# Kernel optimization log

Measured on AMD Instinct MI355X. Metric: run time of the kernel, lower is better.

The kernel has to match this reference:

```python
import jax
import jax.numpy as jnp
import numpy as np
from jax import lax

TAU = 1.0
EPS = 1e-20


def setup_inputs() -> dict:
    key = jax.random.key(0)
    ks = jax.random.split(key, 8)
    B, n, M, G = 256, 128, 512, 512  # batch, seq, mem_size, global dim
    SLOTS = 15                        # his_mem slots (mem_slots - 1)
    d_q = M + G
    his_mem = jax.random.normal(ks[0], (B, SLOTS, M), dtype=jnp.float32)
    states = jax.random.normal(ks[1], (B, n, M), dtype=jnp.float32)
    states_mask = jnp.round(jax.random.uniform(ks[2], (B, n), dtype=jnp.float32))
    global_trace = jax.random.normal(ks[3], (B, G), dtype=jnp.float32)
    null_mem = jnp.zeros((B, 1, M), dtype=jnp.float32)
    gumbel_u = jax.random.uniform(ks[4], (B, n, SLOTS + 1), dtype=jnp.float32)
    attn_W = jax.random.normal(ks[5], (M, d_q + M), dtype=jnp.float32) * 0.02
    attn_b = jax.random.normal(ks[6], (M,), dtype=jnp.float32) * 0.02
    stdv = 1.0 / np.sqrt(M)
    v = jax.random.normal(ks[7], (M,), dtype=jnp.float32) * stdv
    return {"his_mem": his_mem, "states": states, "states_mask": states_mask,
            "global_trace": global_trace, "null_mem": null_mem,
            "gumbel_u": gumbel_u, "attn_W": attn_W, "attn_b": attn_b, "v": v}


def _gumbel_softmax_hard(logits, u, tau):
    # deterministic gumbel noise from uniform samples u in [0,1)
    g = -jnp.log(-jnp.log(jnp.clip(u, EPS, 1.0)) + EPS)
    y_soft = jax.nn.softmax((logits + g) / tau, axis=-1)
    y_hard = jax.nn.one_hot(jnp.argmax(y_soft, axis=-1), logits.shape[-1],
                            dtype=y_soft.dtype)
    # straight-through estimator (matches torch F.gumbel_softmax hard=True)
    return y_hard - lax.stop_gradient(y_soft) + y_soft


def _forward(his_mem, states, states_mask, global_trace, null_mem,
             gumbel_u, attn_W, attn_b, v):
    B, n, M = states.shape
    S = his_mem.shape[1] + 1  # mem_slots (including null slot)

    def step(hm, xs):
        state, mask, u = xs  # [B,M], [B], [B,S]
        mem = jnp.concatenate([hm, null_mem], axis=1)          # [B,S,M]
        query = jnp.concatenate([state, global_trace], axis=1)  # [B,d_q]
        q = jnp.broadcast_to(query[:, None, :], (B, S, query.shape[-1]))
        energy = jnp.tanh(jnp.concatenate([q, mem], axis=2) @ attn_W.T + attn_b)
        attn_energies = energy @ v                              # [B,S]
        attn_weights = jax.nn.softmax(attn_energies, axis=-1)
        empty_mask = (jnp.sum(jnp.abs(mem), axis=-1) == 0).astype(attn_weights.dtype)
        attn_weights = attn_weights + empty_mask * 10.0
        slot_select = _gumbel_softmax_hard(attn_weights, u, TAU)  # [B,S]
        write_mask = (slot_select[:, : S - 1] * mask[:, None])[:, :, None]  # [B,S-1,1]
        hm = (1.0 - write_mask) * hm + write_mask * state[:, None, :]
        return hm, slot_select

    xs = (jnp.swapaxes(states, 0, 1),        # [n,B,M]
          jnp.swapaxes(states_mask, 0, 1),   # [n,B]
          jnp.swapaxes(gumbel_u, 0, 1))      # [n,B,S]
    hm_final, log = lax.scan(step, his_mem, xs)
    write_log = jnp.swapaxes(log, 0, 1)      # [B,n,S]
    return hm_final, write_log


def reference(his_mem, states, states_mask, global_trace, null_mem,
              gumbel_u, attn_W, attn_b, v):
    return _forward(his_mem, states, states_mask, global_trace, null_mem,
                    gumbel_u, attn_W, attn_b, v)
```

## Files before the change

kernel.cpp:

```cpp
#include <hip/hip_runtime.h>

constexpr int kB = 256;
constexpr int kN = 128;
constexpr int kM = 512;
constexpr int kSlots = 15;
constexpr int kS = 16;
constexpr int kW = 1536;
constexpr int kCap = 8192;

__device__ __forceinline__ float tanh_fast(float x)
{
    float xc = fminf(15.f, fmaxf(-15.f, x));
    float ex = __expf(2.f * xc);
    return 1.f - 2.f * __builtin_amdgcn_rcpf(ex + 1.f);
}

__global__ __launch_bounds__(256) void prep1_k(
    const float* __restrict__ his_mem, const float* __restrict__ null_mem,
    const float* __restrict__ gumbel_u, float* __restrict__ out,
    int* __restrict__ empty0, int* __restrict__ cnt, int* __restrict__ total,
    unsigned* __restrict__ list, int* __restrict__ listPos,
    int* __restrict__ ambBatch, unsigned char* __restrict__ amb_flags)
{
    const int b = blockIdx.x;
    const int tid = threadIdx.x;
    const int wave = tid >> 6, lane = tid & 63;
    __shared__ int eflag[kS];
    float* out_hm = out;
    float* out_log = out + (size_t)kB * kSlots * kM;

    for (int s = wave; s < kS; s += 4) {
        const float* p = (s < kSlots) ? his_mem + (size_t)(b * kSlots + s) * kM
                                      : null_mem + (size_t)b * kM;
        float4 v0 = *(const float4*)(p + lane * 4);
        float4 v1 = *(const float4*)(p + 256 + lane * 4);
        int nz = (v0.x != 0.f) | (v0.y != 0.f) | (v0.z != 0.f) | (v0.w != 0.f) |
                 (v1.x != 0.f) | (v1.y != 0.f) | (v1.z != 0.f) | (v1.w != 0.f);
        unsigned long long bal = __ballot(nz);
        if (lane == 0) eflag[s] = (bal == 0ull) ? 1 : 0;
        if (s < kSlots) {
            float* dst = out_hm + (size_t)(b * kSlots + s) * kM;
            *(float4*)(dst + lane * 4) = v0;
            *(float4*)(dst + 256 + lane * 4) = v1;
        }
    }
    __syncthreads();
    if (tid < kS) empty0[b * kS + tid] = eflag[tid];

    if (tid < kN) {
        const int idx = b * kN + tid;
        const float* up = gumbel_u + (size_t)idx * kS;
        float g[kS];
#pragma unroll
        for (int s = 0; s < kS; ++s) {
            float u = fminf(fmaxf(up[s], 1e-20f), 1.0f);
            g[s] = -logf(-logf(u) + 1e-20f);
        }
        float rhs = g[15] + 10.f * (eflag[15] ? 1.f : 0.f) - 1.01f;
        bool amb = false;
#pragma unroll
        for (int s = 0; s < kSlots; ++s)
            amb = amb || (g[s] + 10.f * (eflag[s] ? 1.f : 0.f) >= rhs);
        amb_flags[idx] = amb ? 1 : 0;
        if (amb) {
            int pos = atomicAdd(&total[0], 1);
            if (pos < kCap) list[pos] = (unsigned)idx;
            listPos[idx] = pos;
            int prev = atomicAdd(&cnt[b], 1);
            if (prev == 0) {
                int bp = atomicAdd(&total[1], 1);
                ambBatch[bp] = b;
            }
        }
        float* lp = out_log + (size_t)idx * kS;
        float4 zz = make_float4(0.f, 0.f, 0.f, 0.f);
        *(float4*)(lp + 0) = zz;
        *(float4*)(lp + 4) = zz;
        *(float4*)(lp + 8) = zz;
        *(float4*)(lp + 12) = make_float4(0.f, 0.f, 0.f, 1.f);
    }
}

__global__ __launch_bounds__(256) void prep2_k(
    const float* __restrict__ W, const float* __restrict__ his_mem,
    const float* __restrict__ null_mem, const float* __restrict__ states,
    const float* __restrict__ global_trace, const float* __restrict__ attn_b,
    const int* __restrict__ total, const int* __restrict__ ambBatch,
    const unsigned* __restrict__ list, float* __restrict__ C0,
    float* __restrict__ qCache, float* __restrict__ cwCache,
    int* __restrict__ stepNz)
{
    const int tid = threadIdx.x;

    if (blockIdx.x < 512) {
        const int nab = total[1];
        const int cx = blockIdx.x >> 3;
        const int cy = blockIdx.x & 7;
        if (cx * 4 >= nab) return;
        __shared__ float As[16 * 68];
        __shared__ float Bs[16 * 68];
        const int n0 = cy * 64;
        const int row_l = tid >> 2;
        const int k4 = (tid & 3) * 4;
        const int ty = tid >> 4, tx = tid & 15;

        int bi = cx * 4 + (row_l >> 4);
        if (bi >= nab) bi = nab - 1;
        const int b = ambBatch[bi];
        const int s = row_l & 15;
        const float* ap = (s < kSlots) ? (his_mem + (size_t)(b * kSlots + s) * kM)
                                       : (null_mem + (size_t)b * kM);
        const float* wp = W + (size_t)(n0 + row_l) * kW + 1024;

        float acc[4][4];
#pragma unroll
        for (int i = 0; i < 4; ++i)
#pragma unroll
            for (int j = 0; j < 4; ++j) acc[i][j] = 0.f;

        for (int kt = 0; kt < kM; kt += 16) {
            float4 a4 = *(const float4*)(ap + kt + k4);
            float4 b4 = *(const float4*)(wp + kt + k4);
            __syncthreads();
            As[(k4 + 0) * 68 + row_l] = a4.x; As[(k4 + 1) * 68 + row_l] = a4.y;
            As[(k4 + 2) * 68 + row_l] = a4.z; As[(k4 + 3) * 68 + row_l] = a4.w;
            Bs[(k4 + 0) * 68 + row_l] = b4.x; Bs[(k4 + 1) * 68 + row_l] = b4.y;
            Bs[(k4 + 2) * 68 + row_l] = b4.z; Bs[(k4 + 3) * 68 + row_l] = b4.w;
            __syncthreads();
#pragma unroll
            for (int k = 0; k < 16; ++k) {
                const float4 av = *(const float4*)&As[k * 68 + ty * 4];
                const float4 bv = *(const float4*)&Bs[k * 68 + tx * 4];
                acc[0][0] = fmaf(av.x, bv.x, acc[0][0]);
                acc[0][1] = fmaf(av.x, bv.y, acc[0][1]);
                acc[0][2] = fmaf(av.x, bv.z, acc[0][2]);
                acc[0][3] = fmaf(av.x, bv.w, acc[0][3]);
                acc[1][0] = fmaf(av.y, bv.x, acc[1][0]);
                acc[1][1] = fmaf(av.y, bv.y, acc[1][1]);
                acc[1][2] = fmaf(av.y, bv.z, acc[1][2]);
                acc[1][3] = fmaf(av.y, bv.w, acc[1][3]);
                acc[2][0] = fmaf(av.z, bv.x, acc[2][0]);
                acc[2][1] = fmaf(av.z, bv.y, acc[2][1]);
                acc[2][2] = fmaf(av.z, bv.z, acc[2][2]);
                acc[2][3] = fmaf(av.z, bv.w, acc[2][3]);
                acc[3][0] = fmaf(av.w, bv.x, acc[3][0]);
                acc[3][1] = fmaf(av.w, bv.y, acc[3][1]);
                acc[3][2] = fmaf(av.w, bv.z, acc[3][2]);
                acc[3][3] = fmaf(av.w, bv.w, acc[3][3]);
            }
        }
#pragma unroll
        for (int i = 0; i < 4; ++i) {
            int rl = ty * 4 + i;
            int bij = cx * 4 + (rl >> 4);
            if (bij >= nab) bij = nab - 1;
            int ro = ambBatch[bij] * kS + (rl & 15);
            float4 o = make_float4(acc[i][0], acc[i][1], acc[i][2], acc[i][3]);
            *(float4*)(C0 + (size_t)ro * kM + n0 + tx * 4) = o;
        }
    } else {
        int n = total[0];
        if (n > kCap) n = kCap;
        __shared__ float Xs[1024];
        __shared__ int nzs;

        for (int c = (int)blockIdx.x - 512; c < n * 16; c += 2048) {
            const int i = c >> 4;
            const int j = c & 15;
            const int idx = (int)list[i];
            const int b = idx >> 7;
            __syncthreads();
            if (tid == 0) nzs = 0;
            __syncthreads();
            float s0 = states[(size_t)idx * kM + tid];
            float s1 = states[(size_t)idx * kM + 256 + tid];
            Xs[tid] = s0; Xs[256 + tid] = s1;
            Xs[512 + tid] = global_trace[(size_t)b * kM + tid];
            Xs[768 + tid] = global_trace[(size_t)b * kM + 256 + tid];
            if (s0 != 0.f || s1 != 0.f) nzs = 1;
            __syncthreads();

            const int g = tid >> 4;
            const int l = tid & 15;
#pragma unroll
            for (int p = 0; p < 2; ++p) {
                const int r = j * 32 + p * 16 + g;
                const float* wr = W + (size_t)r * kW;
                float accq = 0.f, accc = 0.f;
#pragma unroll
                for (int jj = 0; jj < 16; ++jj) {
                    int k = l * 4 + jj * 64;
                    float4 w4 = *(const float4*)(wr + k);
                    float4 x4 = *(const float4*)&Xs[k];
                    accq = fmaf(w4.x, x4.x, accq); accq = fmaf(w4.y, x4.y, accq);
                    accq = fmaf(w4.z, x4.z, accq); accq = fmaf(w4.w, x4.w, accq);
                }
#pragma unroll
                for (int jj = 0; jj < 8; ++jj) {
                    int k = l * 4 + jj * 64;
                    float4 w4 = *(const float4*)(wr + 1024 + k);
                    float4 x4 = *(const float4*)&Xs[k];
                    accc = fmaf(w4.x, x4.x, accc); accc = fmaf(w4.y, x4.y, accc);
                    accc = fmaf(w4.z, x4.z, accc); accc = fmaf(w4.w, x4.w, accc);
                }
                accq += __shfl_xor(accq, 1); accq += __shfl_xor(accq, 2);
                accq += __shfl_xor(accq, 4); accq += __shfl_xor(accq, 8);
                accc += __shfl_xor(accc, 1); accc += __shfl_xor(accc, 2);
                accc += __shfl_xor(accc, 4); accc += __shfl_xor(accc, 8);
                if (l == 0) {
                    qCache[(size_t)i * kM + r] = accq + attn_b[r];
                    cwCache[(size_t)i * kM + r] = accc;
                }
            }
            if (tid == 0 && j == 0) stepNz[i] = nzs;
        }
    }
}

constexpr int kCsStride = 528;

__global__ __launch_bounds__(256) void phaseB_k(
    const float* __restrict__ C0, const int* __restrict__ empty0,
    const unsigned char* __restrict__ amb_flags, const int* __restrict__ cnt,
    const int* __restrict__ listPos, const float* __restrict__ qCache,
    const float* __restrict__ cwCache, const int* __restrict__ stepNz,
    const float* __restrict__ states, const float* __restrict__ states_mask,
    const float* __restrict__ gumbel_u, const float* __restrict__ global_trace,
    const float* __restrict__ W, const float* __restrict__ attn_b,
    const float* __restrict__ v, float* __restrict__ out)
{
    const int b = blockIdx.x;
    if (cnt[b] == 0) return;
    const int tid = threadIdx.x;
    float* out_hm = out;
    float* out_log = out + (size_t)kB * kSlots * kM;

    __shared__ float Cs[kS * kCsStride];
    __shared__ float Xb[1024];
    __shared__ float Qb[kM];
    __shared__ float vs[kM];
    __shared__ float e_sh[kS];
    __shared__ float empty_sh[kS];
    __shared__ unsigned char flS[kN];
    __shared__ int slot_src[kSlots];
    __shared__ int k_sh, wk_sh, nz_sh;

    for (int i = tid; i < kS * kM; i += 256) {
        int s = i >> 9, m = i & 511;
        Cs[s * kCsStride + m] = C0[(size_t)(b * kS + s) * kM + m];
    }
    for (int i = tid; i < kM; i += 256) {
        vs[i] = v[i];
        Xb[512 + i] = global_trace[(size_t)b * kM + i];
    }
    if (tid < kS) empty_sh[tid] = empty0[b * kS + tid] ? 1.0f : 0.0f;
    if (tid < kSlots) slot_src[tid] = -1;
    if (tid < kN) flS[tid] = amb_flags[b * kN + tid];
    __syncthreads();

    const int sidx = tid >> 4;
    const int ml = tid & 15;

    for (int t = 0; t < kN; ++t) {
        if (!flS[t]) continue;

        const int pos = listPos[b * kN + t];
        const float* qp;
        if (pos < kCap) {
            qp = qCache + (size_t)pos * kM;
        } else {
            Xb[tid] = states[(size_t)(b * kN + t) * kM + tid];
            Xb[256 + tid] = states[(size_t)(b * kN + t) * kM + 256 + tid];
            __syncthreads();
            const int g2 = tid >> 4, l2 = tid & 15;
            for (int r0 = 0; r0 < kM; r0 += 16) {
                int r = r0 + g2;
                const float* wr = W + (size_t)r * kW;
                float a = 0.f;
                for (int k = l2 * 4; k < 1024; k += 64) {
                    float4 w4 = *(const float4*)(wr + k);
                    float4 x4 = *(const float4*)&Xb[k];
                    a = fmaf(w4.x, x4.x, a); a = fmaf(w4.y, x4.y, a);
                    a = fmaf(w4.z, x4.z, a); a = fmaf(w4.w, x4.w, a);
                }
                a += __shfl_xor(a, 1); a += __shfl_xor(a, 2);
                a += __shfl_xor(a, 4); a += __shfl_xor(a, 8);
                if (l2 == 0) Qb[r] = a + attn_b[r];
            }
            __syncthreads();
            qp = Qb;
        }

        const float* crow = &Cs[sidx * kCsStride];
        float acc = 0.f;
#pragma unroll
        for (int j = 0; j < 8; ++j) {
            int m = ml * 4 + j * 64;
            float4 q4 = *(const float4*)(qp + m);
            float4 c4 = *(const float4*)&crow[m];
            float4 v4 = *(const float4*)&vs[m];
            acc = fmaf(v4.x, tanh_fast(q4.x + c4.x), acc);
            acc = fmaf(v4.y, tanh_fast(q4.y + c4.y), acc);
            acc = fmaf(v4.z, tanh_fast(q4.z + c4.z), acc);
            acc = fmaf(v4.w, tanh_fast(q4.w + c4.w), acc);
        }
        acc += __shfl_xor(acc, 1); acc += __shfl_xor(acc, 2);
        acc += __shfl_xor(acc, 4); acc += __shfl_xor(acc, 8);
        if (ml == 0) e_sh[sidx] = acc;
        __syncthreads();

        if (tid < 64) {
            int s = tid;
            float ev = (s < kS) ? e_sh[s] : -3.0e38f;
            float mx = ev;
            mx = fmaxf(mx, __shfl_xor(mx, 1));
            mx = fmaxf(mx, __shfl_xor(mx, 2));
            mx = fmaxf(mx, __shfl_xor(mx, 4));
            mx = fmaxf(mx, __shfl_xor(mx, 8));
            float w = (s < kS) ? __expf(ev - mx) : 0.f;
            float sm = w;
            sm += __shfl_xor(sm, 1); sm += __shfl_xor(sm, 2);
            sm += __shfl_xor(sm, 4); sm += __shfl_xor(sm, 8);
            w = w / sm;
            w += 10.0f * ((s < kS) ? empty_sh[s] : 0.f);
            float z;
            if (s < kS) {
                float u = gumbel_u[(size_t)(b * kN + t) * kS + s];
                u = fminf(fmaxf(u, 1e-20f), 1.0f);
                float g = -logf(-logf(u) + 1e-20f);
                z = w + g;
            } else z = -3.0e38f;
            float zm = z;
            zm = fmaxf(zm, __shfl_xor(zm, 1));
            zm = fmaxf(zm, __shfl_xor(zm, 2));
            zm = fmaxf(zm, __shfl_xor(zm, 4));
            zm = fmaxf(zm, __shfl_xor(zm, 8));
            unsigned long long bal = __ballot(z == zm) & 0xFFFFull;
            if (s == 0) k_sh = __ffsll(bal) - 1;
        }
        __syncthreads();

        const int k = k_sh;
        if (tid < kS) out_log[(size_t)(b * kN + t) * kS + tid] = (tid == k) ? 1.f : 0.f;
        if (tid == 0) {
            float mv = states_mask[b * kN + t];
            wk_sh = (k < kSlots && mv != 0.0f) ? k : -1;
            nz_sh = 0;
        }
        __syncthreads();

        const int wk = wk_sh;
        if (wk >= 0) {
            if (pos < kCap) {
                Cs[wk * kCsStride + tid] = cwCache[(size_t)pos * kM + tid];
                Cs[wk * kCsStride + 256 + tid] = cwCache[(size_t)pos * kM + 256 + tid];
                if (tid == 0) {
                    slot_src[wk] = t;
                    empty_sh[wk] = stepNz[pos] ? 0.f : 1.f;
                }
            } else {
                if (Xb[tid] != 0.f || Xb[256 + tid] != 0.f) nz_sh = 1;
                __syncthreads();
                const int g2 = tid >> 4, l2 = tid & 15;
                for (int r0 = 0; r0 < kM; r0 += 16) {
                    int r = r0 + g2;
                    const float* wr = W + (size_t)r * kW + 1024;
                    float ca = 0.f;
                    for (int k2 = l2 * 4; k2 < kM; k2 += 64) {
                        float4 w4 = *(const float4*)(wr + k2);
                        float4 x4 = *(const float4*)&Xb[k2];
                        ca = fmaf(w4.x, x4.x, ca); ca = fmaf(w4.y, x4.y, ca);
                        ca = fmaf(w4.z, x4.z, ca); ca = fmaf(w4.w, x4.w, ca);
                    }
                    ca += __shfl_xor(ca, 1); ca += __shfl_xor(ca, 2);
                    ca += __shfl_xor(ca, 4); ca += __shfl_xor(ca, 8);
                    if (l2 == 0) Cs[wk * kCsStride + r] = ca;
                }
                __syncthreads();
                if (tid == 0) {
                    slot_src[wk] = t;
                    empty_sh[wk] = nz_sh ? 0.f : 1.f;
                }
            }
        }
        __syncthreads();
    }

    for (int s = 0; s < kSlots; ++s) {
        int ts = slot_src[s];
        if (ts >= 0) {
            float* dst = out_hm + (size_t)(b * kSlots + s) * kM;
            dst[tid] = states[(size_t)(b * kN + ts) * kM + tid];
            dst[tid + 256] = states[(size_t)(b * kN + ts) * kM + tid + 256];
        }
    }
}

extern "C" void kernel_launch(void* const* d_in, const int* in_sizes, int n_in,
                              void* d_out, int out_size, void* d_ws, size_t ws_size,
                              hipStream_t stream)
{
    const float* his_mem      = (const float*)d_in[0];
    const float* states       = (const float*)d_in[1];
    const float* states_mask  = (const float*)d_in[2];
    const float* global_trace = (const float*)d_in[3];
    const float* null_mem     = (const float*)d_in[4];
    const float* gumbel_u     = (const float*)d_in[5];
    const float* attn_W       = (const float*)d_in[6];
    const float* attn_b       = (const float*)d_in[7];
    const float* v            = (const float*)d_in[8];

    float* C0 = (float*)d_ws;
    float* qCache = C0 + (size_t)kB * kS * kM;
    float* cwCache = qCache + (size_t)kCap * kM;
    int* cnt = (int*)(cwCache + (size_t)kCap * kM);
    int* total = cnt + kB;
    int* empty0 = total + 16;
    int* ambBatch = empty0 + kB * kS;
    int* stepNz = ambBatch + kB;
    int* listPos = stepNz + kCap;
    unsigned* list = (unsigned*)(listPos + kB * kN);
    unsigned char* amb = (unsigned char*)(list + kB * kN);

    hipMemsetAsync(cnt, 0, (kB + 16) * sizeof(int), stream);
    prep1_k<<<kB, 256, 0, stream>>>(his_mem, null_mem, gumbel_u, (float*)d_out,
                                    empty0, cnt, total, list, listPos, ambBatch,
                                    amb);
    prep2_k<<<2560, 256, 0, stream>>>(attn_W, his_mem, null_mem, states,
                                      global_trace, attn_b, total, ambBatch,
                                      list, C0, qCache, cwCache, stepNz);
    phaseB_k<<<kB, 256, 0, stream>>>(C0, empty0, amb, cnt, listPos, qCache,
                                     cwCache, stepNz, states, states_mask,
                                     gumbel_u, global_trace, attn_W, attn_b, v,
                                     (float*)d_out);
}
```

Baseline: 170.4 us.

## Fuse three kernels into one persistent kernel with grid barriers

```diff
diff --git a/kernel.cpp b/kernel.cpp
--- a/kernel.cpp
+++ b/kernel.cpp
@@ -7,6 +7,10 @@
 constexpr int kS = 16;
 constexpr int kW = 1536;
 constexpr int kCap = 8192;
+constexpr int kMaxA = 128;
+constexpr int kGrid = 512;
+constexpr int kCsStride = 528;
+constexpr int kBarStride = 16;
 
 __device__ __forceinline__ float tanh_fast(float x)
 {
@@ -15,169 +19,236 @@
     return 1.f - 2.f * __builtin_amdgcn_rcpf(ex + 1.f);
 }
 
-__global__ __launch_bounds__(256) void prep1_k(
-    const float* __restrict__ his_mem, const float* __restrict__ null_mem,
-    const float* __restrict__ gumbel_u, float* __restrict__ out,
-    int* __restrict__ empty0, int* __restrict__ cnt, int* __restrict__ total,
-    unsigned* __restrict__ list, int* __restrict__ listPos,
-    int* __restrict__ ambBatch, unsigned char* __restrict__ amb_flags)
+__device__ __forceinline__ void grid_barrier(unsigned* bar, unsigned phase)
 {
-    const int b = blockIdx.x;
+    __syncthreads();
+    if (threadIdx.x < 64) {
+        if (threadIdx.x == 0) {
+            __threadfence();
+            atomicAdd(&bar[(blockIdx.x & 63) * kBarStride], 1u);
+        }
+        const unsigned tgt = phase * (kGrid / 64);
+        while (__hip_atomic_load(&bar[threadIdx.x * kBarStride],
+                                 __ATOMIC_RELAXED, __HIP_MEMORY_SCOPE_AGENT) < tgt)
+            __builtin_amdgcn_s_sleep(2);
+        __threadfence();
+    }
+    __syncthreads();
+}
+
+__global__ __launch_bounds__(256, 2) void fused_k(
+    const float* __restrict__ his_mem, const float* __restrict__ states,
+    const float* __restrict__ states_mask, const float* __restrict__ global_trace,
+    const float* __restrict__ null_mem, const float* __restrict__ gumbel_u,
+    const float* __restrict__ W, const float* __restrict__ attn_b,
+    const float* __restrict__ v, float* __restrict__ out, float* __restrict__ C0,
+    float* __restrict__ qCache, float* __restrict__ cwCache,
+    int* __restrict__ cnt_g, int* __restrict__ ambT_g, int* __restrict__ stepNz,
+    unsigned* __restrict__ bar)
+{
     const int tid = threadIdx.x;
-    const int wave = tid >> 6, lane = tid & 63;
-    __shared__ int eflag[kS];
+    const int bid = blockIdx.x;
+
+    __shared__ __align__(16) float SCR[10496];
+    __shared__ float empty_p[kS];
+    __shared__ unsigned char ambList_p[kMaxA];
+    __shared__ int Pex_p[kB + 1];
+    __shared__ short ambBatch_p[kB];
+    __shared__ int wcnt_p[2];
+    __shared__ int cntLoc_p, nab_p, T_p, Pb_p;
+    __shared__ float e_sh[kS];
+    __shared__ int slot_src[kSlots];
+    __shared__ int k_sh, wk_sh, nz_sh;
+
     float* out_hm = out;
     float* out_log = out + (size_t)kB * kSlots * kM;
 
-    for (int s = wave; s < kS; s += 4) {
-        const float* p = (s < kSlots) ? his_mem + (size_t)(b * kSlots + s) * kM
-                                      : null_mem + (size_t)b * kM;
-        float4 v0 = *(const float4*)(p + lane * 4);
-        float4 v1 = *(const float4*)(p + 256 + lane * 4);
-        int nz = (v0.x != 0.f) | (v0.y != 0.f) | (v0.z != 0.f) | (v0.w != 0.f) |
-                 (v1.x != 0.f) | (v1.y != 0.f) | (v1.z != 0.f) | (v1.w != 0.f);
-        unsigned long long bal = __ballot(nz);
-        if (lane == 0) eflag[s] = (bal == 0ull) ? 1 : 0;
-        if (s < kSlots) {
-            float* dst = out_hm + (size_t)(b * kSlots + s) * kM;
-            *(float4*)(dst + lane * 4) = v0;
-            *(float4*)(dst + 256 + lane * 4) = v1;
-        }
-    }
-    __syncthreads();
-    if (tid < kS) empty0[b * kS + tid] = eflag[tid];
-
-    if (tid < kN) {
-        const int idx = b * kN + tid;
-        const float* up = gumbel_u + (size_t)idx * kS;
-        float g[kS];
-#pragma unroll
-        for (int s = 0; s < kS; ++s) {
-            float u = fminf(fmaxf(up[s], 1e-20f), 1.0f);
-            g[s] = -logf(-logf(u) + 1e-20f);
-        }
-        float rhs = g[15] + 10.f * (eflag[15] ? 1.f : 0.f) - 1.01f;
+    if (bid < kB) {
+        const int b = bid;
+        const int wave = tid >> 6, lane = tid & 63;
+        for (int s = wave; s < kS; s += 4) {
+            const float* p = (s < kSlots) ? his_mem + (size_t)(b * kSlots + s) * kM
+                                          : null_mem + (size_t)b * kM;
+            float4 v0 = *(const float4*)(p + lane * 4);
+            float4 v1 = *(const float4*)(p + 256 + lane * 4);
+            int nz = (v0.x != 0.f) | (v0.y != 0.f) | (v0.z != 0.f) | (v0.w != 0.f) |
+                     (v1.x != 0.f) | (v1.y != 0.f) | (v1.z != 0.f) | (v1.w != 0.f);
+            unsigned long long bal = __ballot(nz);
+            if (lane == 0) empty_p[s] = (bal == 0ull) ? 1.f : 0.f;
+            if (s < kSlots) {
+                float* dst = out_hm + (size_t)(b * kSlots + s) * kM;
+                *(float4*)(dst + lane * 4) = v0;
+                *(float4*)(dst + 256 + lane * 4) = v1;
+            }
+        }
+        __syncthreads();
+
         bool amb = false;
-#pragma unroll
-        for (int s = 0; s < kSlots; ++s)
-            amb = amb || (g[s] + 10.f * (eflag[s] ? 1.f : 0.f) >= rhs);
-        amb_flags[idx] = amb ? 1 : 0;
-        if (amb) {
-            int pos = atomicAdd(&total[0], 1);
-            if (pos < kCap) list[pos] = (unsigned)idx;
-            listPos[idx] = pos;
-            int prev = atomicAdd(&cnt[b], 1);
-            if (prev == 0) {
-                int bp = atomicAdd(&total[1], 1);
-                ambBatch[bp] = b;
-            }
-        }
-        float* lp = out_log + (size_t)idx * kS;
-        float4 zz = make_float4(0.f, 0.f, 0.f, 0.f);
-        *(float4*)(lp + 0) = zz;
-        *(float4*)(lp + 4) = zz;
-        *(float4*)(lp + 8) = zz;
-        *(float4*)(lp + 12) = make_float4(0.f, 0.f, 0.f, 1.f);
-    }
-}
-
-__global__ __launch_bounds__(256) void prep2_k(
-    const float* __restrict__ W, const float* __restrict__ his_mem,
-    const float* __restrict__ null_mem, const float* __restrict__ states,
-    const float* __restrict__ global_trace, const float* __restrict__ attn_b,
-    const int* __restrict__ total, const int* __restrict__ ambBatch,
-    const unsigned* __restrict__ list, float* __restrict__ C0,
-    float* __restrict__ qCache, float* __restrict__ cwCache,
-    int* __restrict__ stepNz)
-{
-    const int tid = threadIdx.x;
-
-    if (blockIdx.x < 512) {
-        const int nab = total[1];
-        const int cx = blockIdx.x >> 3;
-        const int cy = blockIdx.x & 7;
-        if (cx * 4 >= nab) return;
-        __shared__ float As[16 * 68];
-        __shared__ float Bs[16 * 68];
-        const int n0 = cy * 64;
-        const int row_l = tid >> 2;
-        const int k4 = (tid & 3) * 4;
-        const int ty = tid >> 4, tx = tid & 15;
-
-        int bi = cx * 4 + (row_l >> 4);
-        if (bi >= nab) bi = nab - 1;
-        const int b = ambBatch[bi];
-        const int s = row_l & 15;
-        const float* ap = (s < kSlots) ? (his_mem + (size_t)(b * kSlots + s) * kM)
-                                       : (null_mem + (size_t)b * kM);
-        const float* wp = W + (size_t)(n0 + row_l) * kW + 1024;
-
-        float acc[4][4];
-#pragma unroll
-        for (int i = 0; i < 4; ++i)
-#pragma unroll
-            for (int j = 0; j < 4; ++j) acc[i][j] = 0.f;
-
-        for (int kt = 0; kt < kM; kt += 16) {
-            float4 a4 = *(const float4*)(ap + kt + k4);
-            float4 b4 = *(const float4*)(wp + kt + k4);
-            __syncthreads();
-            As[(k4 + 0) * 68 + row_l] = a4.x; As[(k4 + 1) * 68 + row_l] = a4.y;
-            As[(k4 + 2) * 68 + row_l] = a4.z; As[(k4 + 3) * 68 + row_l] = a4.w;
-            Bs[(k4 + 0) * 68 + row_l] = b4.x; Bs[(k4 + 1) * 68 + row_l] = b4.y;
-            Bs[(k4 + 2) * 68 + row_l] = b4.z; Bs[(k4 + 3) * 68 + row_l] = b4.w;
-            __syncthreads();
-#pragma unroll
-            for (int k = 0; k < 16; ++k) {
-                const float4 av = *(const float4*)&As[k * 68 + ty * 4];
-                const float4 bv = *(const float4*)&Bs[k * 68 + tx * 4];
-                acc[0][0] = fmaf(av.x, bv.x, acc[0][0]);
-                acc[0][1] = fmaf(av.x, bv.y, acc[0][1]);
-                acc[0][2] = fmaf(av.x, bv.z, acc[0][2]);
-                acc[0][3] = fmaf(av.x, bv.w, acc[0][3]);
-                acc[1][0] = fmaf(av.y, bv.x, acc[1][0]);
-                acc[1][1] = fmaf(av.y, bv.y, acc[1][1]);
-                acc[1][2] = fmaf(av.y, bv.z, acc[1][2]);
-                acc[1][3] = fmaf(av.y, bv.w, acc[1][3]);
-                acc[2][0] = fmaf(av.z, bv.x, acc[2][0]);
-                acc[2][1] = fmaf(av.z, bv.y, acc[2][1]);
-                acc[2][2] = fmaf(av.z, bv.z, acc[2][2]);
-                acc[2][3] = fmaf(av.z, bv.w, acc[2][3]);
-                acc[3][0] = fmaf(av.w, bv.x, acc[3][0]);
-                acc[3][1] = fmaf(av.w, bv.y, acc[3][1]);
-                acc[3][2] = fmaf(av.w, bv.z, acc[3][2]);
-                acc[3][3] = fmaf(av.w, bv.w, acc[3][3]);
-            }
-        }
-#pragma unroll
-        for (int i = 0; i < 4; ++i) {
-            int rl = ty * 4 + i;
-            int bij = cx * 4 + (rl >> 4);
-            if (bij >= nab) bij = nab - 1;
-            int ro = ambBatch[bij] * kS + (rl & 15);
-            float4 o = make_float4(acc[i][0], acc[i][1], acc[i][2], acc[i][3]);
-            *(float4*)(C0 + (size_t)ro * kM + n0 + tx * 4) = o;
+        if (tid < kN) {
+            const int idx = b * kN + tid;
+            const float* up = gumbel_u + (size_t)idx * kS;
+            float g[kS];
+#pragma unroll
+            for (int s = 0; s < kS; ++s) {
+                float u = fminf(fmaxf(up[s], 1e-20f), 1.0f);
+                g[s] = -logf(-logf(u) + 1e-20f);
+            }
+            float rhs = g[15] + 10.f * empty_p[15] - 1.01f;
+#pragma unroll
+            for (int s = 0; s < kSlots; ++s)
+                amb = amb || (g[s] + 10.f * empty_p[s] >= rhs);
+            float* lp = out_log + (size_t)idx * kS;
+            float4 zz = make_float4(0.f, 0.f, 0.f, 0.f);
+            *(float4*)(lp + 0) = zz;
+            *(float4*)(lp + 4) = zz;
+            *(float4*)(lp + 8) = zz;
+            *(float4*)(lp + 12) = make_float4(0.f, 0.f, 0.f, 1.f);
+        }
+        unsigned long long m = __ballot(amb);
+        if (tid < kN && (tid & 63) == 0) wcnt_p[tid >> 6] = __popcll(m);
+        __syncthreads();
+        if (tid < kN && amb) {
+            int base = (tid >= 64) ? wcnt_p[0] : 0;
+            int pos = base + __popcll(m & ((1ull << (tid & 63)) - 1ull));
+            ambList_p[pos] = (unsigned char)tid;
+            ambT_g[b * kMaxA + pos] = tid;
+        }
+        if (tid == 0) {
+            int c = wcnt_p[0] + wcnt_p[1];
+            cntLoc_p = c;
+            cnt_g[b] = c;
         }
     } else {
-        int n = total[0];
-        if (n > kCap) n = kCap;
-        __shared__ float Xs[1024];
-        __shared__ int nzs;
-
-        for (int c = (int)blockIdx.x - 512; c < n * 16; c += 2048) {
+        const float* wp = W + (size_t)(bid - kB) * 3072;
+        float acc = 0.f;
+        for (int i = tid; i < 3072; i += 256) acc += wp[i];
+        asm volatile("" :: "v"(acc));
+    }
+
+    grid_barrier(bar, 1);
+
+    {
+        int* sc  = (int*)(SCR + 3200);
+        int* sc2 = (int*)(SCR + 3456);
+        int cv = cnt_g[tid];
+        int iv = (cv > 0) ? 1 : 0;
+        sc[tid] = cv;
+        sc2[tid] = iv;
+        for (int off = 1; off < kB; off <<= 1) {
+            __syncthreads();
+            int a  = (tid >= off) ? sc[tid - off] : 0;
+            int a2 = (tid >= off) ? sc2[tid - off] : 0;
+            __syncthreads();
+            sc[tid] += a;
+            sc2[tid] += a2;
+        }
+        __syncthreads();
+        Pex_p[tid + 1] = sc[tid];
+        if (iv) ambBatch_p[sc2[tid] - 1] = (short)tid;
+        if (tid == 0) {
+            Pex_p[0] = 0;
+            T_p = sc[kB - 1];
+            nab_p = sc2[kB - 1];
+            Pb_p = (bid > 0 && bid < kB) ? sc[bid - 1] : 0;
+        }
+        __syncthreads();
+    }
+
+    const int nab = nab_p;
+    int Tc = T_p;
+    if (Tc > kCap) Tc = kCap;
+
+    if (nab > 0) {
+        float* As = SCR;
+        float* Bs = SCR + 1088;
+        const int nTiles = ((nab + 3) >> 2) * 8;
+        for (int tile = bid; tile < nTiles; tile += kGrid) {
+            const int cx = tile >> 3;
+            const int cy = tile & 7;
+            const int n0 = cy * 64;
+            const int row_l = tid >> 2;
+            const int k4 = (tid & 3) * 4;
+            const int ty = tid >> 4, tx = tid & 15;
+            int bi = cx * 4 + (row_l >> 4);
+            if (bi >= nab) bi = nab - 1;
+            const int b = ambBatch_p[bi];
+            const int s = row_l & 15;
+            const float* ap = (s < kSlots)
+                                  ? (his_mem + (size_t)(b * kSlots + s) * kM)
+                                  : (null_mem + (size_t)b * kM);
+            const float* wp = W + (size_t)(n0 + row_l) * kW + 1024;
+
+            float acc[4][4];
+#pragma unroll
+            for (int i = 0; i < 4; ++i)
+#pragma unroll
+                for (int j = 0; j < 4; ++j) acc[i][j] = 0.f;
+
+            for (int kt = 0; kt < kM; kt += 16) {
+                float4 a4 = *(const float4*)(ap + kt + k4);
+                float4 b4 = *(const float4*)(wp + kt + k4);
+                __syncthreads();
+                As[(k4 + 0) * 68 + row_l] = a4.x; As[(k4 + 1) * 68 + row_l] = a4.y;
+                As[(k4 + 2) * 68 + row_l] = a4.z; As[(k4 + 3) * 68 + row_l] = a4.w;
+                Bs[(k4 + 0) * 68 + row_l] = b4.x; Bs[(k4 + 1) * 68 + row_l] = b4.y;
+                Bs[(k4 + 2) * 68 + row_l] = b4.z; Bs[(k4 + 3) * 68 + row_l] = b4.w;
+                __syncthreads();
+#pragma unroll
+                for (int k = 0; k < 16; ++k) {
+                    const float4 av = *(const float4*)&As[k * 68 + ty * 4];
+                    const float4 bv = *(const float4*)&Bs[k * 68 + tx * 4];
+                    acc[0][0] = fmaf(av.x, bv.x, acc[0][0]);
+                    acc[0][1] = fmaf(av.x, bv.y, acc[0][1]);
+                    acc[0][2] = fmaf(av.x, bv.z, acc[0][2]);
+                    acc[0][3] = fmaf(av.x, bv.w, acc[0][3]);
+                    acc[1][0] = fmaf(av.y, bv.x, acc[1][0]);
+                    acc[1][1] = fmaf(av.y, bv.y, acc[1][1]);
+                    acc[1][2] = fmaf(av.y, bv.z, acc[1][2]);
+                    acc[1][3] = fmaf(av.y, bv.w, acc[1][3]);
+                    acc[2][0] = fmaf(av.z, bv.x, acc[2][0]);
+                    acc[2][1] = fmaf(av.z, bv.y, acc[2][1]);
+                    acc[2][2] = fmaf(av.z, bv.z, acc[2][2]);
+                    acc[2][3] = fmaf(av.z, bv.w, acc[2][3]);
+                    acc[3][0] = fmaf(av.w, bv.x, acc[3][0]);
+                    acc[3][1] = fmaf(av.w, bv.y, acc[3][1]);
+                    acc[3][2] = fmaf(av.w, bv.z, acc[3][2]);
+                    acc[3][3] = fmaf(av.w, bv.w, acc[3][3]);
+                }
+            }
+#pragma unroll
+            for (int i = 0; i < 4; ++i) {
+                int rl = ty * 4 + i;
+                int bij = cx * 4 + (rl >> 4);
+                if (bij >= nab) bij = nab - 1;
+                int ro = (int)ambBatch_p[bij] * kS + (rl & 15);
+                float4 o = make_float4(acc[i][0], acc[i][1], acc[i][2], acc[i][3]);
+                *(float4*)(C0 + (size_t)ro * kM + n0 + tx * 4) = o;
+            }
+        }
+    }
+
+    {
+        float* Xs = SCR + 2176;
+        for (int c = bid; c < Tc * 16; c += kGrid) {
             const int i = c >> 4;
             const int j = c & 15;
-            const int idx = (int)list[i];
-            const int b = idx >> 7;
-            __syncthreads();
-            if (tid == 0) nzs = 0;
+            int lo = 0, hi = kB - 1;
+            while (lo < hi) {
+                int mid = (lo + hi + 1) >> 1;
+                if (Pex_p[mid] <= i) lo = mid; else hi = mid - 1;
+            }
+            const int b = lo;
+            const int t = ambT_g[b * kMaxA + (i - Pex_p[b])];
+            const int idx = b * kN + t;
+            __syncthreads();
+            if (tid == 0) nz_sh = 0;
             __syncthreads();
             float s0 = states[(size_t)idx * kM + tid];
             float s1 = states[(size_t)idx * kM + 256 + tid];
             Xs[tid] = s0; Xs[256 + tid] = s1;
             Xs[512 + tid] = global_trace[(size_t)b * kM + tid];
             Xs[768 + tid] = global_trace[(size_t)b * kM + 256 + tid];
-            if (s0 != 0.f || s1 != 0.f) nzs = 1;
+            if (s0 != 0.f || s1 != 0.f) nz_sh = 1;
             __syncthreads();
 
             const int g = tid >> 4;
@@ -212,59 +283,40 @@
                     cwCache[(size_t)i * kM + r] = accc;
                 }
             }
-            if (tid == 0 && j == 0) stepNz[i] = nzs;
-        }
-    }
-}
-
-constexpr int kCsStride = 528;
-
-__global__ __launch_bounds__(256) void phaseB_k(
-    const float* __restrict__ C0, const int* __restrict__ empty0,
-    const unsigned char* __restrict__ amb_flags, const int* __restrict__ cnt,
-    const int* __restrict__ listPos, const float* __restrict__ qCache,
-    const float* __restrict__ cwCache, const int* __restrict__ stepNz,
-    const float* __restrict__ states, const float* __restrict__ states_mask,
-    const float* __restrict__ gumbel_u, const float* __restrict__ global_trace,
-    const float* __restrict__ W, const float* __restrict__ attn_b,
-    const float* __restrict__ v, float* __restrict__ out)
-{
-    const int b = blockIdx.x;
-    if (cnt[b] == 0) return;
-    const int tid = threadIdx.x;
-    float* out_hm = out;
-    float* out_log = out + (size_t)kB * kSlots * kM;
-
-    __shared__ float Cs[kS * kCsStride];
-    __shared__ float Xb[1024];
-    __shared__ float Qb[kM];
-    __shared__ float vs[kM];
-    __shared__ float e_sh[kS];
-    __shared__ float empty_sh[kS];
-    __shared__ unsigned char flS[kN];
-    __shared__ int slot_src[kSlots];
-    __shared__ int k_sh, wk_sh, nz_sh;
+            if (tid == 0 && j == 0) stepNz[i] = nz_sh;
+        }
+    }
+
+    grid_barrier(bar, 2);
+
+    if (bid >= kB) return;
+    const int b = bid;
+    const int cnt = cntLoc_p;
+    if (cnt == 0) return;
+
+    float* Cs  = SCR;
+    float* vsd = SCR + 8448;
+    float* Xb  = SCR + 8960;
+    float* Qb  = SCR + 9984;
 
     for (int i = tid; i < kS * kM; i += 256) {
-        int s = i >> 9, m = i & 511;
-        Cs[s * kCsStride + m] = C0[(size_t)(b * kS + s) * kM + m];
+        int s = i >> 9, mcol = i & 511;
+        Cs[s * kCsStride + mcol] = C0[(size_t)(b * kS + s) * kM + mcol];
     }
     for (int i = tid; i < kM; i += 256) {
-        vs[i] = v[i];
+        vsd[i] = v[i];
         Xb[512 + i] = global_trace[(size_t)b * kM + i];
     }
-    if (tid < kS) empty_sh[tid] = empty0[b * kS + tid] ? 1.0f : 0.0f;
     if (tid < kSlots) slot_src[tid] = -1;
-    if (tid < kN) flS[tid] = amb_flags[b * kN + tid];
     __syncthreads();
 
     const int sidx = tid >> 4;
     const int ml = tid & 15;
-
-    for (int t = 0; t < kN; ++t) {
-        if (!flS[t]) continue;
-
-        const int pos = listPos[b * kN + t];
+    const int Pb = Pb_p;
+
+    for (int jj = 0; jj < cnt; ++jj) {
+        const int t = ambList_p[jj];
+        const int pos = Pb + jj;
         const float* qp;
         if (pos < kCap) {
             qp = qCache + (size_t)pos * kM;
@@ -295,10 +347,10 @@
         float acc = 0.f;
 #pragma unroll
         for (int j = 0; j < 8; ++j) {
-            int m = ml * 4 + j * 64;
-            float4 q4 = *(const float4*)(qp + m);
-            float4 c4 = *(const float4*)&crow[m];
-            float4 v4 = *(const float4*)&vs[m];
+            int mcol = ml * 4 + j * 64;
+            float4 q4 = *(const float4*)(qp + mcol);
+            float4 c4 = *(const float4*)&crow[mcol];
+            float4 v4 = *(const float4*)&vsd[mcol];
             acc = fmaf(v4.x, tanh_fast(q4.x + c4.x), acc);
             acc = fmaf(v4.y, tanh_fast(q4.y + c4.y), acc);
             acc = fmaf(v4.z, tanh_fast(q4.z + c4.z), acc);
@@ -322,7 +374,7 @@
             sm += __shfl_xor(sm, 1); sm += __shfl_xor(sm, 2);
             sm += __shfl_xor(sm, 4); sm += __shfl_xor(sm, 8);
             w = w / sm;
-            w += 10.0f * ((s < kS) ? empty_sh[s] : 0.f);
+            w += 10.0f * ((s < kS) ? empty_p[s] : 0.f);
             float z;
             if (s < kS) {
                 float u = gumbel_u[(size_t)(b * kN + t) * kS + s];
@@ -341,7 +393,8 @@
         __syncthreads();
 
         const int k = k_sh;
-        if (tid < kS) out_log[(size_t)(b * kN + t) * kS + tid] = (tid == k) ? 1.f : 0.f;
+        if (tid < kS)
+            out_log[(size_t)(b * kN + t) * kS + tid] = (tid == k) ? 1.f : 0.f;
         if (tid == 0) {
             float mv = states_mask[b * kN + t];
             wk_sh = (k < kSlots && mv != 0.0f) ? k : -1;
@@ -356,7 +409,7 @@
                 Cs[wk * kCsStride + 256 + tid] = cwCache[(size_t)pos * kM + 256 + tid];
                 if (tid == 0) {
                     slot_src[wk] = t;
-                    empty_sh[wk] = stepNz[pos] ? 0.f : 1.f;
+                    empty_p[wk] = stepNz[pos] ? 0.f : 1.f;
                 }
             } else {
                 if (Xb[tid] != 0.f || Xb[256 + tid] != 0.f) nz_sh = 1;
@@ -379,7 +432,7 @@
                 __syncthreads();
                 if (tid == 0) {
                     slot_src[wk] = t;
-                    empty_sh[wk] = nz_sh ? 0.f : 1.f;
+                    empty_p[wk] = nz_sh ? 0.f : 1.f;
                 }
             }
         }
@@ -413,24 +466,14 @@
     float* C0 = (float*)d_ws;
     float* qCache = C0 + (size_t)kB * kS * kM;
     float* cwCache = qCache + (size_t)kCap * kM;
-    int* cnt = (int*)(cwCache + (size_t)kCap * kM);
-    int* total = cnt + kB;
-    int* empty0 = total + 16;
-    int* ambBatch = empty0 + kB * kS;
-    int* stepNz = ambBatch + kB;
-    int* listPos = stepNz + kCap;
-    unsigned* list = (unsigned*)(listPos + kB * kN);
-    unsigned char* amb = (unsigned char*)(list + kB * kN);
-
-    hipMemsetAsync(cnt, 0, (kB + 16) * sizeof(int), stream);
-    prep1_k<<<kB, 256, 0, stream>>>(his_mem, null_mem, gumbel_u, (float*)d_out,
-                                    empty0, cnt, total, list, listPos, ambBatch,
-                                    amb);
-    prep2_k<<<2560, 256, 0, stream>>>(attn_W, his_mem, null_mem, states,
-                                      global_trace, attn_b, total, ambBatch,
-                                      list, C0, qCache, cwCache, stepNz);
-    phaseB_k<<<kB, 256, 0, stream>>>(C0, empty0, amb, cnt, listPos, qCache,
-                                     cwCache, stepNz, states, states_mask,
-                                     gumbel_u, global_trace, attn_W, attn_b, v,
-                                     (float*)d_out);
+    int* cnt_g = (int*)(cwCache + (size_t)kCap * kM);
+    int* ambT_g = cnt_g + kB;
+    int* stepNz = ambT_g + kB * kMaxA;
+    unsigned* bar = (unsigned*)(stepNz + kCap);
+
+    hipMemsetAsync(bar, 0, 64 * kBarStride * sizeof(unsigned), stream);
+    fused_k<<<kGrid, 256, 0, stream>>>(his_mem, states, states_mask,
+                                       global_trace, null_mem, gumbel_u, attn_W,
+                                       attn_b, v, (float*)d_out, C0, qCache,
+                                       cwCache, cnt_g, ambT_g, stepNz, bar);
 }
```

Result: slower. 214.0 us (+25.5%).
